# Performance work log

Hardware: AMD Instinct MI355X
Metric: run time of the kernel (lower is better)

The kernel has to match this reference:

```python
import jax, jax.numpy as jnp
import numpy as np

NEG = jnp.float32(-1e30)   # stand-in for -inf (keeps grads NaN-free)
DUP = jnp.float32(-2e30)   # mask for duplicate (merged-away) candidates


def ctc_prefix_beam_search(logits, beam_size, blank_index):
    """Vectorized CTC prefix beam search, faithful to the torch `beams` fn.
    Prefixes are fixed-length int32 token arrays padded with -1 (bijective
    encoding of the original strings since alphabet chars are unique).
    Returns (scores=[B] logaddexp(pb,pnb), prefixes=[B,T], lengths=[B])."""
    T, V = logits.shape
    B = beam_size
    K = beam_size  # torch code takes top-beam_size symbols per frame
    ctc = jax.nn.log_softmax(logits, axis=-1)  # [T,V] log-probs
    pos = jnp.arange(T)

    # initial beam: one empty hypothesis, rest are -inf dummies with unique
    # sentinel first tokens so they never merge with real prefixes
    prefixes = jnp.full((B, T), -1, jnp.int32)
    sent = -(jnp.arange(B, dtype=jnp.int32) + 2)
    prefixes = prefixes.at[:, 0].set(jnp.where(jnp.arange(B) == 0, -1, sent))
    lengths = jnp.zeros((B,), jnp.int32)
    pb = jnp.full((B,), NEG, jnp.float32).at[0].set(0.0)   # ends-in-blank logp
    pnb = jnp.full((B,), NEG, jnp.float32)                 # ends-in-nonblank logp

    def step(carry, logp):
        prefixes, lengths, pb, pnb = carry
        ps, s = jax.lax.top_k(logp, K)                     # [K] values, indices
        is_blank = (s == blank_index)[None, :]             # [1,K]
        last = jnp.where(lengths > 0,
                         prefixes[jnp.arange(B), jnp.maximum(lengths - 1, 0)],
                         -1)                               # [B] last token or -1
        same = last[:, None] == s[None, :]                 # [B,K]
        pb_ps = pb[:, None] + ps[None, :]
        pnb_ps = pnb[:, None] + ps[None, :]
        both = jnp.logaddexp(pb_ps, pnb_ps)

        # group 1: prefix unchanged (blank emission, or repeat of last symbol)
        g1_pb = jnp.where(is_blank, both, NEG)
        g1_pnb = jnp.where(same & ~is_blank, pnb_ps, NEG)
        g1_prefix = jnp.broadcast_to(prefixes[:, None, :], (B, K, T))
        g1_len = jnp.broadcast_to(lengths[:, None], (B, K))

        # group 2: prefix extended by s (non-blank only; blank rows get NEG)
        g2_pnb = jnp.where(is_blank, NEG, jnp.where(same, pb_ps, both))
        g2_pb = jnp.full((B, K), NEG, jnp.float32)
        g2_prefix = jnp.where(pos[None, None, :] == lengths[:, None, None],
                              s[None, :, None], prefixes[:, None, :])
        g2_len = g1_len + 1

        C = 2 * B * K
        cand_prefix = jnp.concatenate([g1_prefix, g2_prefix]).reshape(C, T)
        cand_len = jnp.concatenate([g1_len, g2_len]).reshape(C)
        cand_pb = jnp.concatenate([g1_pb, g2_pb]).reshape(C)
        cand_pnb = jnp.concatenate([g1_pnb, g2_pnb]).reshape(C)

        # merge candidates with identical prefixes (the dict logsumexp in torch)
        eq = jnp.all(cand_prefix[:, None, :] == cand_prefix[None, :, :], axis=-1)
        merged_pb = jax.nn.logsumexp(jnp.where(eq, cand_pb[None, :], NEG), axis=1)
        merged_pnb = jax.nn.logsumexp(jnp.where(eq, cand_pnb[None, :], NEG), axis=1)
        first = jnp.argmax(eq, axis=1) == jnp.arange(C)    # keep first occurrence
        total = jnp.logaddexp(merged_pb, merged_pnb)
        _, idx = jax.lax.top_k(jnp.where(first, total, DUP), B)

        return (cand_prefix[idx], cand_len[idx], merged_pb[idx], merged_pnb[idx]), None

    (prefixes, lengths, pb, pnb), _ = jax.lax.scan(
        step, (prefixes, lengths, pb, pnb), ctc)
    scores = jnp.logaddexp(pb, pnb)
    return scores, prefixes, lengths


def setup_inputs() -> dict:
    key = jax.random.key(0)
    T, V = 200, 29
    logits = jax.random.normal(key, (T, V), dtype=jnp.float32)
    return {"logits": logits, "beam_size": 10, "blank_index": 28}


def reference(logits, beam_size, blank_index):
    return ctc_prefix_beam_search(logits, beam_size, blank_index)
```

## Files before the change

### kernel.cpp

```cpp
#include <hip/hip_runtime.h>
#include <math.h>


#define BB 10
#define KK 10
#define VV 29
#define TMAX 256
#define FS 56
#define NEGF (-1e30f)
#define DUPF (-2e30f)
#define MAGICF 0x5CA7F00Du
#define SENTB 0x7F800000
#define NHEAT 255

__device__ __forceinline__ float lae(float a, float b) {
    float m = fmaxf(a, b);
    return m + log1pf(expf(fminf(a, b) - m));
}
__device__ __forceinline__ unsigned int ordf(float f) {
    unsigned int u = __float_as_uint(f);
    return (u & 0x80000000u) ? ~u : (u | 0x80000000u);
}

__device__ __forceinline__ void topk_frame(const float* __restrict__ logits,
                                           int blank, int t, float* __restrict__ o,
                                           int L) {
    float lp = (L < VV) ? logits[t * VV + L] : -INFINITY;
    float mx = lp;
    #pragma unroll
    for (int off = 32; off >= 1; off >>= 1) mx = fmaxf(mx, __shfl_xor(mx, off));
    float sm = (L < VV) ? expf(lp - mx) : 0.f;
    #pragma unroll
    for (int off = 32; off >= 1; off >>= 1) sm += __shfl_xor(sm, off);
    float lz = mx + logf(sm);
    int arank = 0;
    #pragma unroll
    for (int u = 0; u < VV; ++u) {
        float lu = __shfl(lp, u);
        arank += (lu > lp) || (lu == lp && u < L);
    }
    bool win = (L < VV) && (arank < KK);
    if (win) { o[2 * arank] = __int_as_float(L); o[2 * arank + 1] = lp - lz; }
    if (L < 32) o[24 + L] = win ? (lp - lz) : __int_as_float(SENTB);
    unsigned long long bm = __ballot(win && (L == blank));
    if (bm) { if (L == blank) { o[20] = __int_as_float(arank); o[21] = lp - lz; } }
    else    { if (L == 0)     { o[20] = __int_as_float(-1);    o[21] = 0.f;     } }
}

__global__ __launch_bounds__(192) void fused_kernel(
        const float* __restrict__ logits, const int* __restrict__ blank_p,
        float* __restrict__ out, int T, float* __restrict__ tkbuf,
        unsigned int* fflags) {

    const int L = threadIdx.x;

    if (blockIdx.x != 0) {
        if ((int)blockIdx.x <= T) {
            const int t = blockIdx.x - 1;
            if (L < 64) topk_frame(logits, blank_p[0], t, tkbuf + t * FS, L);
            __syncthreads();
            if (L == 0)
                __hip_atomic_store(&fflags[t], MAGICF, __ATOMIC_RELEASE,
                                   __HIP_MEMORY_SCOPE_AGENT);
            return;
        }
        float a0 = (float)L * 0.5f + 1.0f, a1 = a0 + 0.25f;
        float a2 = a0 + 0.5f,              a3 = a0 + 0.75f;
        unsigned long long t0 = __builtin_amdgcn_s_memrealtime();
        for (;;) {
            if (__hip_atomic_load(&fflags[T], __ATOMIC_RELAXED,
                                  __HIP_MEMORY_SCOPE_AGENT) == MAGICF) break;
            if (__builtin_amdgcn_s_memrealtime() - t0 > 300000ull) break;
            #pragma unroll
            for (int i = 0; i < 256; ++i) {
                a0 = fmaf(a0, 1.0000002f, 1e-7f);
                a1 = fmaf(a1, 1.0000002f, 1e-7f);
                a2 = fmaf(a2, 1.0000002f, 1e-7f);
                a3 = fmaf(a3, 1.0000002f, 1e-7f);
            }
        }
        asm volatile("" :: "v"(a0), "v"(a1), "v"(a2), "v"(a3));
        return;
    }

    __builtin_amdgcn_s_setprio(3);

    __shared__ __align__(16) float tkl[TMAX * FS];
    __shared__ __align__(16) float bsrow[16][8];
    __shared__ __align__(16) int   dupsig[12];
    __shared__ __align__(16) unsigned long long kbuf[128];
    __shared__ __align__(16) float4 aux4[12];
    __shared__ unsigned short hist[TMAX][BB];
    __shared__ signed char pout[BB][TMAX];

    if (L < BB) {
        int last0 = (L == 0) ? -1 : -(L + 2);
        int par0  = (L == 0) ? -1 : 0;
        int f2 = (last0 + 16) | ((par0 + 1) << 8) | ((-1 + 16) << 16);
        *(float4*)&bsrow[L][0] = make_float4((L == 0) ? 0.f : NEGF, NEGF,
                                             __int_as_float(f2), __int_as_float(0));
        *(float4*)&bsrow[L][4] = make_float4(0.f, NEGF, __int_as_float(SENTB), 0.f);
        dupsig[L] = f2 & 0xFFFF;
    } else if (L < 12) dupsig[L] = 0;

    if (L < 64) {
        for (;;) {
            bool ok = true;
            for (int base = 0; base < T; base += 64) {
                int idx = base + L;
                unsigned f = (idx < T)
                    ? __hip_atomic_load(&fflags[idx], __ATOMIC_RELAXED,
                                        __HIP_MEMORY_SCOPE_AGENT)
                    : MAGICF;
                ok = ok && (f == MAGICF);
            }
            if (__all(ok)) break;
        }
    }
    __syncthreads();
    __builtin_amdgcn_fence(__ATOMIC_ACQUIRE, "agent");

    {
        int n4 = (T * FS) >> 2;
        const float4* g4 = (const float4*)tkbuf;
        float4* l4 = (float4*)tkl;
        for (int i = L; i < n4; i += 192) l4[i] = g4[i];
    }
    __syncthreads();

    const int w  = L >> 6;
    const int wl = L & 63;
    const bool isg1 = (w == 2) && (wl < BB);
    const bool isg2 = (w == 0) ? (wl < 54) : ((w == 1) ? (wl < 46) : false);
    const bool active = isg1 || isg2;
    const bool isshadow = (w == 0) ? (wl >= 54) : ((w == 1) && wl >= 46 && wl < 56);
    const int shb = (w == 0) ? (wl - 54) : (wl - 46);
    const int c = isg1 ? wl : ((w == 0) ? (L + 10) : L);
    const int b = isg1 ? c : (c - 10) / 10;
    const int k = isg1 ? 0 : (c - 10) % 10;
    const int ofs = isg1 ? 20 : (isg2 ? 2 * k : 20);
    const int blank = blank_p[0];

    float2 fpr = *(const float2*)&tkl[ofs];

    for (int t = 0; t < T; ++t) {
        float tot = -INFINITY, pay_pb = NEGF, pay_pnb = NEGF;
        int nlen = 0, nlast = 0, xsl = -1, tok = -1;

        if (active) {
            float4 rowA = *(const float4*)&bsrow[b][0];
            int f2 = __float_as_int(rowA.z);
            int last_b = (f2 & 255) - 16;
            if (isg1) {
                float4 rowB = *(const float4*)&bsrow[b][4];
                int par_b  = ((f2 >> 8) & 255) - 1;
                int last_p = ((f2 >> 16) & 255) - 16;
                nlen = __float_as_int(rowA.w);
                nlast = last_b; xsl = par_b; tok = -1;
                int bk = __float_as_int(fpr.x);
                float pbl = fpr.y;
                float pkl = rowB.z;
                if (bk >= 0) pay_pb = lae(rowA.x + pbl, rowA.y + pbl);
                if (__float_as_int(rowB.z) != SENTB) {
                    float a = rowA.y + pkl;
                    if (par_b >= 0) {
                        float e = (last_b == last_p) ? (rowB.x + pkl)
                                   : lae(rowB.x + pkl, rowB.y + pkl);
                        float mxx = fmaxf(a, e);
                        pay_pnb = mxx + logf(expf(a - mxx) + expf(e - mxx));
                    } else pay_pnb = a;
                }
                tot = lae(pay_pb, pay_pnb);
            } else {
                int s = __float_as_int(fpr.x); float p = fpr.y;
                nlen = __float_as_int(rowA.w) + 1;
                nlast = s; xsl = b; tok = s;
                int4 dg0 = *(const int4*)&dupsig[0];
                int4 dg1 = *(const int4*)&dupsig[4];
                int2 dg2 = *(const int2*)&dupsig[8];
                int sig[BB] = {dg0.x, dg0.y, dg0.z, dg0.w,
                               dg1.x, dg1.y, dg1.z, dg1.w, dg2.x, dg2.y};
                int target = ((b + 1) << 8) | (s + 16);
                bool dup = false;
                #pragma unroll
                for (int i = 0; i < BB; ++i) dup = dup || (sig[i] == target);
                float v;
                if (s == blank)        v = NEGF;
                else if (s == last_b)  v = rowA.x + p;
                else                   v = lae(rowA.x + p, rowA.y + p);
                pay_pnb = v;
                tot = dup ? DUPF : v;
            }
        }

        unsigned long long key =
            (((unsigned long long)ordf(tot)) << 32) | (unsigned)(127 - c);
        if (active) kbuf[c] = key;
        if (isg1)   aux4[c] = make_float4(pay_pb, pay_pnb,
                                          __int_as_float(nlast + 16), 0.f);
        __syncthreads();

        if (isshadow) key = kbuf[shb];

        int tn = (t + 1 < T) ? (t + 1) : t;
        const float* tkn = &tkl[tn * FS];
        fpr = *(const float2*)&tkn[ofs];

        int r = 0;
        const ulonglong2* k2 = (const ulonglong2*)kbuf;
        #pragma unroll
        for (int q = 0; q < 55; ++q) {
            ulonglong2 w2 = k2[q];
            r += (w2.x > key) + (w2.y > key);
        }

        int g1r_val = ((isg1 || isshadow) && r < BB) ? r : -1;
        int xs = (xsl < 0) ? 0 : xsl;
        int src = (w == 0) ? (54 + xs) : ((w == 1) ? (46 + xs) : xs);
        int g1r_sh = __shfl(g1r_val, src);

        if (active && r < BB) {
            float4 ax = aux4[xs];
            int npar, plast16; float ppb, ppnb;
            if (xsl >= 0) {
                npar = g1r_sh; plast16 = __float_as_int(ax.z);
                ppb = ax.x; ppnb = ax.y;
            } else { npar = -1; plast16 = 15; ppb = 0.f; ppnb = NEGF; }
            int li = ((unsigned)nlast < VV) ? nlast : 29;
            float npkl = tkn[24 + li];
            int f2n = (nlast + 16) | ((npar + 1) << 8) | (plast16 << 16);
            *(float4*)&bsrow[r][0] = make_float4(isg1 ? pay_pb : NEGF, pay_pnb,
                                                 __int_as_float(f2n),
                                                 __int_as_float(nlen));
            *(float4*)&bsrow[r][4] = make_float4(ppb, ppnb, npkl, 0.f);
            dupsig[r] = f2n & 0xFFFF;
            hist[t][r] = (unsigned short)(b | ((tok + 1) << 8));
        }
        __syncthreads();
    }

    int mylen = 0;
    if (L < BB) {
        float4 rj = *(const float4*)&bsrow[L][0];
        mylen = __float_as_int(rj.w);
        out[L] = lae(rj.x, rj.y);
        out[BB + BB * T + L] = (float)mylen;
    }
    for (int i = L; i < BB * TMAX; i += 192) (&pout[0][0])[i] = -1;
    __syncthreads();
    if (L < BB) {
        int cur = L, pos = mylen - 1;
        for (int tt = T - 1; tt >= 0; --tt) {
            unsigned short h = hist[tt][cur];
            int tk2 = (h >> 8) - 1;
            if (tk2 >= 0) pout[L][pos--] = (signed char)tk2;
            cur = h & 255;
        }
        if (mylen == 0 && cur > 0) pout[L][0] = (signed char)(-(cur + 2));
    }
    __syncthreads();
    for (int e = L; e < BB * T; e += 192) {
        int j = e / T, p = e - j * T;
        out[BB + e] = (float)pout[j][p];
    }

    if (L == 0)
        __hip_atomic_store(&fflags[T], MAGICF, __ATOMIC_RELEASE,
                           __HIP_MEMORY_SCOPE_AGENT);
}

extern "C" void kernel_launch(void* const* d_in, const int* in_sizes, int n_in,
                              void* d_out, int out_size, void* d_ws, size_t ws_size,
                              hipStream_t stream) {
    const float* logits = (const float*)d_in[0];
    const int* blank_p = (const int*)d_in[2];
    int T = in_sizes[0] / VV;
    float* tkbuf = (float*)d_ws;

    size_t ff_off = ((size_t)T * FS * 4 + 255) & ~(size_t)255;
    unsigned int* fflags = (unsigned int*)((char*)d_ws + ff_off);

    fused_kernel<<<dim3(1 + T + NHEAT), dim3(192), 0, stream>>>(
        logits, blank_p, (float*)d_out, T, tkbuf, fflags);
}
```

Before: 440.1 us.

## Materialize beam prefixes incrementally in double-buffered strings instead of backtracking history

Drops the per-frame history table and the serial end-of-scan backtrack. Wave 2, which used to idle during the rank count, now copies the previous frame's prefix strings into a double buffer, using the per-slot parent and token record kept in histcu. The group-1 (unchanged-prefix) slot writes move to shadow lanes that take their key and metadata from the aux4 entry. This removes a sequential T-step backtrack at the tail but adds shared-memory copy traffic every frame, and it assumes a prefix length of at most 208.

```diff
diff --git a/kernel.cpp b/kernel.cpp
--- a/kernel.cpp
+++ b/kernel.cpp
@@ -90,8 +90,10 @@
     __shared__ __align__(16) int   dupsig[12];
     __shared__ __align__(16) unsigned long long kbuf[128];
     __shared__ __align__(16) float4 aux4[12];
-    __shared__ unsigned short hist[TMAX][BB];
-    __shared__ signed char pout[BB][TMAX];
+    __shared__ __align__(16) unsigned histcu[2][16];
+    __shared__ __align__(16) signed char strbuf[2][BB][208];
+
+    for (int i = L; i < 520; i += 192) ((int*)strbuf)[i] = -1;
 
     if (L < BB) {
         int last0 = (L == 0) ? -1 : -(L + 2);
@@ -125,6 +127,7 @@
         const float4* g4 = (const float4*)tkbuf;
         float4* l4 = (float4*)tkl;
         for (int i = L; i < n4; i += 192) l4[i] = g4[i];
+        if (L >= 1 && L < BB) strbuf[0][L][0] = (signed char)(-(L + 2));
     }
     __syncthreads();
 
@@ -193,75 +196,138 @@
             }
         }
 
+        unsigned ordmine = ordf(tot);
         unsigned long long key =
-            (((unsigned long long)ordf(tot)) << 32) | (unsigned)(127 - c);
+            (((unsigned long long)ordmine) << 32) | (unsigned)(127 - c);
         if (active) kbuf[c] = key;
-        if (isg1)   aux4[c] = make_float4(pay_pb, pay_pnb,
-                                          __int_as_float(nlast + 16), 0.f);
+        if (isg1) {
+            int meta = (nlast + 16) | (nlen << 6) | ((xsl + 1) << 14);
+            aux4[c] = make_float4(pay_pb, pay_pnb, __int_as_float(meta),
+                                  __int_as_float((int)ordmine));
+        }
         __syncthreads();
 
-        if (isshadow) key = kbuf[shb];
+        float4 ax0 = make_float4(0.f, 0.f, 0.f, 0.f);
+        float4 axp = make_float4(0.f, 0.f, 0.f, 0.f);
+        int xsl_s = -1;
+        if (isshadow) {
+            ax0 = *(const float4*)&aux4[shb];
+            key = (((unsigned long long)(unsigned)__float_as_int(ax0.w)) << 32)
+                  | (unsigned)(127 - shb);
+            int meta = __float_as_int(ax0.z);
+            xsl_s = ((meta >> 14) & 15) - 1;
+            if (w == 0 && xsl_s >= 0) axp = *(const float4*)&aux4[xsl_s];
+        }
 
         int tn = (t + 1 < T) ? (t + 1) : t;
         const float* tkn = &tkl[tn * FS];
         fpr = *(const float2*)&tkn[ofs];
 
-        int r = 0;
-        const ulonglong2* k2 = (const ulonglong2*)kbuf;
-        #pragma unroll
-        for (int q = 0; q < 55; ++q) {
-            ulonglong2 w2 = k2[q];
-            r += (w2.x > key) + (w2.y > key);
-        }
-
-        int g1r_val = ((isg1 || isshadow) && r < BB) ? r : -1;
-        int xs = (xsl < 0) ? 0 : xsl;
-        int src = (w == 0) ? (54 + xs) : ((w == 1) ? (46 + xs) : xs);
+        int r = 255;
+        if (w < 2) {
+            int rr = 0;
+            const ulonglong2* k2 = (const ulonglong2*)kbuf;
+            #pragma unroll
+            for (int q = 0; q < 55; ++q) {
+                ulonglong2 w2 = k2[q];
+                rr += (w2.x > key) + (w2.y > key);
+            }
+            r = rr;
+        } else if (t > 0) {
+            int kprev = t - 1;
+            int pr = kprev & 1, pw = pr ^ 1;
+            #pragma unroll
+            for (int it = 0; it < 3; ++it) {
+                int chunk = wl + 64 * it;
+                if (chunk < 130) {
+                    int row = chunk / 13, c16 = chunk - row * 13;
+                    if (c16 * 16 <= kprev) {
+                        int srcrow = (int)(histcu[pr][row] & 15u);
+                        *(float4*)&strbuf[pw][row][c16 * 16] =
+                            *(const float4*)&strbuf[pr][srcrow][c16 * 16];
+                    }
+                }
+            }
+            if (wl < BB) {
+                unsigned hc = histcu[pr][wl];
+                int tokp1 = (int)((hc >> 8) & 255u);
+                int lenr  = (int)(hc >> 16);
+                if (tokp1) strbuf[pw][wl][lenr - 1] = (signed char)(tokp1 - 1);
+            }
+        }
+
+        int xs = isshadow ? ((xsl_s < 0) ? 0 : xsl_s) : ((b < BB) ? b : 0);
+        int g1r_val = (isshadow && r < BB) ? r : -1;
+        int src = (w == 0) ? (54 + xs) : (46 + xs);
         int g1r_sh = __shfl(g1r_val, src);
 
-        if (active && r < BB) {
+        if (isg2 && r < BB) {
             float4 ax = aux4[xs];
-            int npar, plast16; float ppb, ppnb;
-            if (xsl >= 0) {
-                npar = g1r_sh; plast16 = __float_as_int(ax.z);
-                ppb = ax.x; ppnb = ax.y;
-            } else { npar = -1; plast16 = 15; ppb = 0.f; ppnb = NEGF; }
+            int npar = g1r_sh;
+            int plast16 = __float_as_int(ax.z) & 63;
+            float ppb = ax.x, ppnb = ax.y;
             int li = ((unsigned)nlast < VV) ? nlast : 29;
             float npkl = tkn[24 + li];
             int f2n = (nlast + 16) | ((npar + 1) << 8) | (plast16 << 16);
-            *(float4*)&bsrow[r][0] = make_float4(isg1 ? pay_pb : NEGF, pay_pnb,
+            *(float4*)&bsrow[r][0] = make_float4(NEGF, pay_pnb,
                                                  __int_as_float(f2n),
                                                  __int_as_float(nlen));
             *(float4*)&bsrow[r][4] = make_float4(ppb, ppnb, npkl, 0.f);
             dupsig[r] = f2n & 0xFFFF;
-            hist[t][r] = (unsigned short)(b | ((tok + 1) << 8));
+            histcu[t & 1][r] = (unsigned)(b | ((tok + 1) << 8) | (nlen << 16));
+        }
+        if (w == 0 && isshadow && r < BB) {
+            int meta = __float_as_int(ax0.z);
+            int nlast_s = (meta & 63) - 16;
+            int nlen_s  = (meta >> 6) & 255;
+            int li = ((unsigned)nlast_s < VV) ? nlast_s : 29;
+            float npkl = tkn[24 + li];
+            int npar, plast16; float ppb, ppnb;
+            if (xsl_s >= 0) {
+                npar = g1r_sh; plast16 = __float_as_int(axp.z) & 63;
+                ppb = axp.x; ppnb = axp.y;
+            } else { npar = -1; plast16 = 15; ppb = 0.f; ppnb = NEGF; }
+            int f2n = (nlast_s + 16) | ((npar + 1) << 8) | (plast16 << 16);
+            *(float4*)&bsrow[r][0] = make_float4(ax0.x, ax0.y,
+                                                 __int_as_float(f2n),
+                                                 __int_as_float(nlen_s));
+            *(float4*)&bsrow[r][4] = make_float4(ppb, ppnb, npkl, 0.f);
+            dupsig[r] = f2n & 0xFFFF;
+            histcu[t & 1][r] = (unsigned)(shb | (nlen_s << 16));
         }
         __syncthreads();
     }
 
-    int mylen = 0;
+    int fin;
+    {
+        int kprev = T - 1, pr = kprev & 1, pw = pr ^ 1;
+        fin = pw;
+        if (L < 130) {
+            int row = L / 13, c16 = L - row * 13;
+            if (c16 * 16 <= kprev) {
+                int srcrow = (int)(histcu[pr][row] & 15u);
+                *(float4*)&strbuf[pw][row][c16 * 16] =
+                    *(const float4*)&strbuf[pr][srcrow][c16 * 16];
+            }
+        }
+        __syncthreads();
+        if (L < BB) {
+            unsigned hc = histcu[pr][L];
+            int tokp1 = (int)((hc >> 8) & 255u);
+            int lenr  = (int)(hc >> 16);
+            if (tokp1) strbuf[pw][L][lenr - 1] = (signed char)(tokp1 - 1);
+        }
+        __syncthreads();
+    }
+
     if (L < BB) {
         float4 rj = *(const float4*)&bsrow[L][0];
-        mylen = __float_as_int(rj.w);
         out[L] = lae(rj.x, rj.y);
-        out[BB + BB * T + L] = (float)mylen;
-    }
-    for (int i = L; i < BB * TMAX; i += 192) (&pout[0][0])[i] = -1;
-    __syncthreads();
-    if (L < BB) {
-        int cur = L, pos = mylen - 1;
-        for (int tt = T - 1; tt >= 0; --tt) {
-            unsigned short h = hist[tt][cur];
-            int tk2 = (h >> 8) - 1;
-            if (tk2 >= 0) pout[L][pos--] = (signed char)tk2;
-            cur = h & 255;
-        }
-        if (mylen == 0 && cur > 0) pout[L][0] = (signed char)(-(cur + 2));
-    }
-    __syncthreads();
+        out[BB + BB * T + L] = (float)__float_as_int(rj.w);
+    }
     for (int e = L; e < BB * T; e += 192) {
         int j = e / T, p = e - j * T;
-        out[BB + e] = (float)pout[j][p];
+        out[BB + e] = (float)strbuf[fin][j][p];
     }
 
     if (L == 0)
```

Result: slower. 451.4 us (+2.6%).
